# Performance work log

Measured on AMD Instinct MI355X. Metric: run time of the kernel, lower is better.

Reference implementation:

```python
import jax, jax.numpy as jnp
import numpy as np

ALPHA = 0.2  # LeakyReLU negative slope
MASK_VAL = -9e15


def setup_inputs() -> dict:
    key = jax.random.key(0)
    k1, k2, k3, k4 = jax.random.split(key, 4)
    B, N, F_IN = 4, 2048, 256
    H, HD = 8, 32  # out_features = H*HD = 256
    x = jax.random.normal(k1, (B, N, F_IN), dtype=jnp.float32)
    adj = jax.random.randint(k2, (B, N, N), 0, 2, dtype=jnp.int32)
    W = jax.random.normal(k3, (H, F_IN, HD), dtype=jnp.float32) * (1.0 / np.sqrt(F_IN))
    a = jax.random.normal(k4, (H, 2 * HD, 1), dtype=jnp.float32) * 0.1
    return {"x": x, "adj": adj, "W": W, "a": a}


def reference(x, adj, W, a):
    # x: (B,N,F), W: (H,F,D), a: (H,2D,1)
    B, N, _ = x.shape
    H, _, D = W.shape
    Wh = jnp.einsum('bnf,hfd->bhnd', x, W)  # (B,H,N,D)
    # Split additive attention vector: cat([Wh_i, Wh_j]) @ a == Wh_i@a1 + Wh_j@a2
    a1 = a[:, :D, 0]   # (H,D)
    a2 = a[:, D:, 0]   # (H,D)
    s1 = jnp.einsum('bhnd,hd->bhn', Wh, a1)  # source scores
    s2 = jnp.einsum('bhnd,hd->bhn', Wh, a2)  # target scores
    e = jax.nn.leaky_relu(s1[:, :, :, None] + s2[:, :, None, :], negative_slope=ALPHA)  # (B,H,N,N)
    e = jnp.where(adj[:, None, :, :] == 0, MASK_VAL, e)
    attention = jax.nn.softmax(e, axis=-1)  # dropout skipped (eval mode)
    h = jnp.einsum('bhij,bhjd->bhid', attention, Wh)  # (B,H,N,D)
    h = jnp.transpose(h, (0, 2, 1, 3)).reshape(B, N, H * D)
    return jax.nn.elu(h)
```

## Files before the change

kernel.cpp:

```cpp
#include <hip/hip_runtime.h>
#include <hip/hip_bf16.h>

#define ALPHA 0.2f

typedef __attribute__((ext_vector_type(8))) short short8;
typedef __attribute__((ext_vector_type(4))) short s4;
typedef __attribute__((ext_vector_type(8))) _Float16 h8;
typedef __attribute__((ext_vector_type(2))) _Float16 h2v;
typedef __attribute__((ext_vector_type(4))) float f32x4;

static constexpr int B = 4, N = 2048, F = 256, H = 8, D = 32;
static constexpr int SZ_X = B * N * F, SZ_ADJ = B * N * N, SZ_W = H * F * D, SZ_A = H * 2 * D;
static const float C1 = 1.4426950408889634f;
static const float C2 = ALPHA * 1.4426950408889634f;


__device__ __forceinline__ unsigned rne16(unsigned u) {
    return u + 0x7fffu + ((u >> 16) & 1u);
}
__device__ __forceinline__ unsigned pk_rne(float a, float b) {
    return __builtin_amdgcn_perm(rne16(__float_as_uint(b)),
                                 rne16(__float_as_uint(a)), 0x07060302u);
}
__device__ __forceinline__ unsigned h2mul(unsigned a, unsigned b) {
    h2v r = __builtin_bit_cast(h2v, a) * __builtin_bit_cast(h2v, b);
    return __builtin_bit_cast(unsigned, r);
}
__device__ __forceinline__ unsigned h2max(unsigned a, unsigned b) {
    h2v r = __builtin_elementwise_max(__builtin_bit_cast(h2v, a),
                                      __builtin_bit_cast(h2v, b));
    return __builtin_bit_cast(unsigned, r);
}
__device__ __forceinline__ unsigned dup16f(float x) {
    unsigned short w = __builtin_bit_cast(unsigned short, (_Float16)x);
    return (unsigned)w | ((unsigned)w << 16);
}

__global__ void k0_prep(const float* __restrict__ Wp, const float* __restrict__ ap,
                        unsigned short* __restrict__ WT2, float* __restrict__ AF) {
    int bid = blockIdx.x;
    int h = bid >> 5, d = bid & 31;
    int f = threadIdx.x;
    unsigned short v = (unsigned short)(rne16(__float_as_uint(Wp[(h * F + f) * D + d])) >> 16);
    WT2[(size_t)(f >> 5) * 8192 + (h * 32 + d) * 32 + (f & 31)] = v;
    if (d == 0 && f < 64) AF[h * 64 + f] = ap[h * 64 + f];
}

__global__ void kbit(const int* __restrict__ adj, unsigned long long* __restrict__ bm) {
    int wid = blockIdx.x * 4 + (threadIdx.x >> 6);
    int lane = threadIdx.x & 63;
    size_t base = (size_t)wid * 16;
#pragma unroll
    for (int s = 0; s < 16; s++) {
        size_t strip = base + s;
        int v = adj[strip * 64 + lane];
        unsigned long long m = __ballot(v != 0);
        if (lane == 0) bm[strip] = m;
    }
}

__global__ __launch_bounds__(256) void k12(const float* __restrict__ x,
                                           const unsigned short* __restrict__ WT2,
                                           const float* __restrict__ AF,
                                           unsigned short* __restrict__ WHT,
                                           float* __restrict__ S1,
                                           _Float16* __restrict__ UH,
                                           _Float16* __restrict__ VH) {
    __shared__ unsigned short XA[16 * 264];
    int bid = blockIdx.x;
    int b = bid >> 7;
    int n0 = (bid & 127) * 16;
    int t = threadIdx.x;
    int wave = t >> 6, lane = t & 63;
    int lm = lane & 15, lq = lane >> 4;

#pragma unroll
    for (int q = 0; q < 4; q++) {
        int idx = q * 256 + t;
        int row = idx >> 6, c16 = idx & 63;
        f32x4 v = *(const f32x4*)(x + (size_t)(b * N + n0 + row) * F + c16 * 4);
        unsigned* dst = (unsigned*)&XA[row * 264 + c16 * 4];
        dst[0] = pk_rne(v[0], v[1]);
        dst[1] = pk_rne(v[2], v[3]);
    }
    __syncthreads();

    f32x4 acc[4] = {};
#pragma unroll
    for (int kc = 0; kc < 8; kc++) {
        short8 afr = *(const short8*)&XA[lm * 264 + kc * 32 + lq * 8];
#pragma unroll
        for (int c = 0; c < 4; c++) {
            int hd = wave * 64 + c * 16 + lm;
            short8 bfr = *(const short8*)(WT2 + (size_t)kc * 8192 + hd * 32 + lq * 8);
            acc[c] = __builtin_amdgcn_mfma_f32_16x16x32_bf16(afr, bfr, acc[c], 0, 0, 0);
        }
    }

#pragma unroll
    for (int c = 0; c < 4; c++) {
        int hd = wave * 64 + c * 16 + lm;
        unsigned short w0 = __builtin_bit_cast(unsigned short, (_Float16)acc[c][0]);
        unsigned short w1 = __builtin_bit_cast(unsigned short, (_Float16)acc[c][1]);
        unsigned short w2 = __builtin_bit_cast(unsigned short, (_Float16)acc[c][2]);
        unsigned short w3 = __builtin_bit_cast(unsigned short, (_Float16)acc[c][3]);
        uint2 pk;
        pk.x = (unsigned)w0 | ((unsigned)w1 << 16);
        pk.y = (unsigned)w2 | ((unsigned)w3 << 16);
        *(uint2*)&WHT[((size_t)b * 256 + hd) * 2048 + n0 + lq * 4] = pk;
    }
#pragma unroll
    for (int cp = 0; cp < 2; cp++) {
        int h = wave * 2 + cp;
        float a1l = AF[h * 64 + lm],      a1h = AF[h * 64 + 16 + lm];
        float a2l = AF[h * 64 + 32 + lm], a2h = AF[h * 64 + 48 + lm];
#pragma unroll
        for (int r = 0; r < 4; r++) {
            float s1p = acc[cp * 2][r] * a1l + acc[cp * 2 + 1][r] * a1h;
            float s2p = acc[cp * 2][r] * a2l + acc[cp * 2 + 1][r] * a2h;
#pragma unroll
            for (int off = 1; off <= 8; off <<= 1) {
                s1p += __shfl_xor(s1p, off);
                s2p += __shfl_xor(s2p, off);
            }
            if (lm == 0) {
                int bh = b * 8 + h, n = n0 + lq * 4 + r;
                S1[(size_t)bh * 2048 + n] = s1p;
                UH[(size_t)bh * 2048 + n] = (_Float16)exp2f(C1 * s2p);
                VH[(size_t)bh * 2048 + n] = (_Float16)exp2f(C2 * s2p);
            }
        }
    }
}

__global__ __launch_bounds__(256) void k3_attn(
    const unsigned* __restrict__ bm32,
    const unsigned short* __restrict__ WHT,
    const float* __restrict__ S1,
    const _Float16* __restrict__ UH, const _Float16* __restrict__ VH,
    float* __restrict__ out) {
    __shared__ unsigned LM[4][32 * 66];
    __shared__ unsigned short LW[2][32 * 140];

    int bid = blockIdx.x;
    int isup = bid & 15;
    int bh = bid >> 4;
    int b = bh >> 3, h = bh & 7;
    int i0 = isup * 128;
    int t = threadIdx.x;
    int wave = t >> 6, lane = t & 63;
    int irow = lane & 15, quad = lane >> 4;
    int iw = i0 + wave * 32;

    {
        unsigned* lm = LM[wave];
        const unsigned* src = bm32 + ((size_t)(b * N + iw)) * 64;
#pragma unroll 4
        for (int r = 0; r < 32; r++)
            lm[r * 66 + lane] = src[(size_t)r * 64 + lane];
    }

    const unsigned short* wsrc = WHT + ((size_t)b * 256 + h * 32) * 2048;
    int srow = t >> 3, sseg = (t & 7) * 16;

    {
        const unsigned short* g = wsrc + (size_t)srow * 2048 + sseg;
        union { short8 v; s4 q[2]; } a, c;
        a.v = *(const short8*)(g);
        c.v = *(const short8*)(g + 8);
        unsigned short* d = &LW[0][srow * 140 + sseg];
        *(s4*)(d) = a.q[0]; *(s4*)(d + 4) = a.q[1];
        *(s4*)(d + 8) = c.q[0]; *(s4*)(d + 12) = c.q[1];
    }

    float s1A = S1[(size_t)bh * 2048 + iw + irow];
    float s1B = S1[(size_t)bh * 2048 + iw + 16 + irow];
    unsigned ci2A = dup16f(exp2f((C2 - C1) * s1A));
    unsigned ci2B = dup16f(exp2f((C2 - C1) * s1B));
    const _Float16* up = UH + (size_t)bh * 2048;
    const _Float16* vp = VH + (size_t)bh * 2048;

    union { h8 v; unsigned u[4]; } ones;
    ones.u[0] = ones.u[1] = ones.u[2] = ones.u[3] = 0x3C003C00u;

    f32x4 aA0 = {0,0,0,0}, aA1 = {0,0,0,0}, aAL = {0,0,0,0};
    f32x4 aB0 = {0,0,0,0}, aB1 = {0,0,0,0}, aBL = {0,0,0,0};
    __syncthreads();

    for (int cc = 0; cc < 16; cc++) {
        union { short8 v; s4 q[2]; } pa, pc;
        if (cc < 15) {
            const unsigned short* g = wsrc + (size_t)srow * 2048 + (cc + 1) * 128 + sseg;
            pa.v = *(const short8*)(g);
            pc.v = *(const short8*)(g + 8);
        }
        const unsigned short* lwp = LW[cc & 1];
        const unsigned* lmw = LM[wave];
#pragma unroll
        for (int ks = 0; ks < 4; ks++) {
            int jl = ks * 32 + quad * 8;
            int jg = cc * 128 + jl;
            uint4 uw = *(const uint4*)(up + jg);
            uint4 vw = *(const uint4*)(vp + jg);
            unsigned mkA = lmw[irow * 66 + cc * 4 + ks] >> (quad * 8);
            unsigned mkB = lmw[(16 + irow) * 66 + cc * 4 + ks] >> (quad * 8);
            unsigned mA0 = ((mkA & 1u)  ? 0x3C00u : 0u) | ((mkA & 2u)   ? 0x3C000000u : 0u);
            unsigned mA1 = ((mkA & 4u)  ? 0x3C00u : 0u) | ((mkA & 8u)   ? 0x3C000000u : 0u);
            unsigned mA2 = ((mkA & 16u) ? 0x3C00u : 0u) | ((mkA & 32u)  ? 0x3C000000u : 0u);
            unsigned mA3 = ((mkA & 64u) ? 0x3C00u : 0u) | ((mkA & 128u) ? 0x3C000000u : 0u);
            unsigned mB0 = ((mkB & 1u)  ? 0x3C00u : 0u) | ((mkB & 2u)   ? 0x3C000000u : 0u);
            unsigned mB1 = ((mkB & 4u)  ? 0x3C00u : 0u) | ((mkB & 8u)   ? 0x3C000000u : 0u);
            unsigned mB2 = ((mkB & 16u) ? 0x3C00u : 0u) | ((mkB & 32u)  ? 0x3C000000u : 0u);
            unsigned mB3 = ((mkB & 64u) ? 0x3C00u : 0u) | ((mkB & 128u) ? 0x3C000000u : 0u);
            union { h8 v; unsigned u[4]; } afA, afB;
            afA.u[0] = h2mul(h2max(uw.x, h2mul(ci2A, vw.x)), mA0);
            afA.u[1] = h2mul(h2max(uw.y, h2mul(ci2A, vw.y)), mA1);
            afA.u[2] = h2mul(h2max(uw.z, h2mul(ci2A, vw.z)), mA2);
            afA.u[3] = h2mul(h2max(uw.w, h2mul(ci2A, vw.w)), mA3);
            afB.u[0] = h2mul(h2max(uw.x, h2mul(ci2B, vw.x)), mB0);
            afB.u[1] = h2mul(h2max(uw.y, h2mul(ci2B, vw.y)), mB1);
            afB.u[2] = h2mul(h2max(uw.z, h2mul(ci2B, vw.z)), mB2);
            afB.u[3] = h2mul(h2max(uw.w, h2mul(ci2B, vw.w)), mB3);
            union { short8 v; s4 q[2]; } bf0, bf1;
            bf0.q[0] = *(const s4*)&lwp[irow * 140 + jl];
            bf0.q[1] = *(const s4*)&lwp[irow * 140 + jl + 4];
            bf1.q[0] = *(const s4*)&lwp[(16 + irow) * 140 + jl];
            bf1.q[1] = *(const s4*)&lwp[(16 + irow) * 140 + jl + 4];
            h8 b0 = __builtin_bit_cast(h8, bf0.v);
            h8 b1 = __builtin_bit_cast(h8, bf1.v);
            aA0 = __builtin_amdgcn_mfma_f32_16x16x32_f16(afA.v, b0, aA0, 0, 0, 0);
            aA1 = __builtin_amdgcn_mfma_f32_16x16x32_f16(afA.v, b1, aA1, 0, 0, 0);
            aAL = __builtin_amdgcn_mfma_f32_16x16x32_f16(afA.v, ones.v, aAL, 0, 0, 0);
            aB0 = __builtin_amdgcn_mfma_f32_16x16x32_f16(afB.v, b0, aB0, 0, 0, 0);
            aB1 = __builtin_amdgcn_mfma_f32_16x16x32_f16(afB.v, b1, aB1, 0, 0, 0);
            aBL = __builtin_amdgcn_mfma_f32_16x16x32_f16(afB.v, ones.v, aBL, 0, 0, 0);
        }
        if (cc < 15) {
            unsigned short* d = &LW[(cc + 1) & 1][srow * 140 + sseg];
            *(s4*)(d) = pa.q[0]; *(s4*)(d + 4) = pa.q[1];
            *(s4*)(d + 8) = pc.q[0]; *(s4*)(d + 12) = pc.q[1];
        }
        __syncthreads();
    }

#pragma unroll
    for (int r = 0; r < 4; r++) {
        float lA = aAL[r], lB = aBL[r];
        float rA = 1.0f / (lA > 0.f ? lA : 1.f);
        float rB = 1.0f / (lB > 0.f ? lB : 1.f);
        float vA0 = aA0[r] * rA, vA1 = aA1[r] * rA;
        float vB0 = aB0[r] * rB, vB1 = aB1[r] * rB;
        vA0 = vA0 > 0.f ? vA0 : __expf(vA0) - 1.f;
        vA1 = vA1 > 0.f ? vA1 : __expf(vA1) - 1.f;
        vB0 = vB0 > 0.f ? vB0 : __expf(vB0) - 1.f;
        vB1 = vB1 > 0.f ? vB1 : __expf(vB1) - 1.f;
        int iA = iw + quad * 4 + r, iB = iA + 16;
        size_t rbA = (size_t)(b * N + iA) * 256 + h * 32;
        size_t rbB = (size_t)(b * N + iB) * 256 + h * 32;
        out[rbA + irow] = vA0;
        out[rbA + 16 + irow] = vA1;
        out[rbB + irow] = vB0;
        out[rbB + 16 + irow] = vB1;
    }
}

extern "C" void kernel_launch(void* const* d_in, const int* in_sizes, int n_in,
                              void* d_out, int out_size, void* d_ws, size_t ws_size,
                              hipStream_t stream) {
    const void *xP = nullptr, *adjP = nullptr, *WP = nullptr, *aP = nullptr;
    for (int i = 0; i < n_in; i++) {
        switch (in_sizes[i]) {
            case SZ_X:   xP = d_in[i]; break;
            case SZ_ADJ: adjP = d_in[i]; break;
            case SZ_W:   WP = d_in[i]; break;
            case SZ_A:   aP = d_in[i]; break;
            default: break;
        }
    }
    if (!xP || !adjP || !WP || !aP) { xP = d_in[0]; adjP = d_in[1]; WP = d_in[2]; aP = d_in[3]; }
    float* out = (float*)d_out;

    char* ws = (char*)d_ws;
    unsigned short* WT2 = (unsigned short*)(ws);
    float* AF  = (float*)(ws + 131072);
    float* S1  = (float*)(ws + 133120);
    _Float16* UH = (_Float16*)(ws + 395264);
    _Float16* VH = (_Float16*)(ws + 526336);
    unsigned short* WHT = (unsigned short*)(ws + 657408);
    unsigned long long* BM = (unsigned long long*)(ws + 4851712);

    k0_prep<<<256, 256, 0, stream>>>((const float*)WP, (const float*)aP, WT2, AF);
    kbit<<<4096, 256, 0, stream>>>((const int*)adjP, BM);
    k12<<<512, 256, 0, stream>>>((const float*)xP, WT2, AF, WHT, S1, UH, VH);
    k3_attn<<<512, 256, 0, stream>>>((const unsigned*)BM, WHT, S1, UH, VH, out);
}
```

Baseline: 155.3 us.

## Fuse adjacency bitmask pass into projection kernel, bitwise mask, remap attention blocks

Merges the adjacency-to-bitmask kernel and the projection/score kernel into a single launch, interleaving eight bitmask blocks with one projection block so the memory-bound and compute-bound work overlap and one launch is saved. In the attention loop, the per-pair mask multiply is replaced by a bitwise AND against a mask built with a multiply and arithmetic shift, which removes several selects and one fp16 multiply per element. The attention block index is remapped so consecutive blocks cover different heads of the same batch, aiming at better L2 reuse of the bitmask rows. The mixed-role grid gives blocks uneven work, which can hurt scheduling balance.

```diff
diff --git a/kernel.cpp b/kernel.cpp
--- a/kernel.cpp
+++ b/kernel.cpp
@@ -8,6 +8,7 @@
 typedef __attribute__((ext_vector_type(8))) _Float16 h8;
 typedef __attribute__((ext_vector_type(2))) _Float16 h2v;
 typedef __attribute__((ext_vector_type(4))) float f32x4;
+typedef __attribute__((ext_vector_type(2))) short sh2;
 
 static constexpr int B = 4, N = 2048, F = 256, H = 8, D = 32;
 static constexpr int SZ_X = B * N * F, SZ_ADJ = B * N * N, SZ_W = H * F * D, SZ_A = H * 2 * D;
@@ -34,6 +35,12 @@
 __device__ __forceinline__ unsigned dup16f(float x) {
     unsigned short w = __builtin_bit_cast(unsigned short, (_Float16)x);
     return (unsigned)w | ((unsigned)w << 16);
+}
+__device__ __forceinline__ unsigned bits2mask(unsigned mk, unsigned mulc) {
+    unsigned w = (mk & 3u) * mulc;
+    sh2 s = __builtin_bit_cast(sh2, w);
+    s = s >> 15;
+    return __builtin_bit_cast(unsigned, s);
 }
 
 __global__ void k0_prep(const float* __restrict__ Wp, const float* __restrict__ ap,
@@ -46,31 +53,37 @@
     if (d == 0 && f < 64) AF[h * 64 + f] = ap[h * 64 + f];
 }
 
-__global__ void kbit(const int* __restrict__ adj, unsigned long long* __restrict__ bm) {
-    int wid = blockIdx.x * 4 + (threadIdx.x >> 6);
-    int lane = threadIdx.x & 63;
-    size_t base = (size_t)wid * 16;
-#pragma unroll
-    for (int s = 0; s < 16; s++) {
-        size_t strip = base + s;
-        int v = adj[strip * 64 + lane];
-        unsigned long long m = __ballot(v != 0);
-        if (lane == 0) bm[strip] = m;
-    }
-}
-
-__global__ __launch_bounds__(256) void k12(const float* __restrict__ x,
-                                           const unsigned short* __restrict__ WT2,
-                                           const float* __restrict__ AF,
-                                           unsigned short* __restrict__ WHT,
-                                           float* __restrict__ S1,
-                                           _Float16* __restrict__ UH,
-                                           _Float16* __restrict__ VH) {
+__global__ __launch_bounds__(256) void k2_fused(const float* __restrict__ x,
+                                                const unsigned short* __restrict__ WT2,
+                                                const float* __restrict__ AF,
+                                                unsigned short* __restrict__ WHT,
+                                                float* __restrict__ S1,
+                                                _Float16* __restrict__ UH,
+                                                _Float16* __restrict__ VH,
+                                                const int* __restrict__ adj,
+                                                unsigned long long* __restrict__ bm) {
     __shared__ unsigned short XA[16 * 264];
     int bid = blockIdx.x;
-    int b = bid >> 7;
-    int n0 = (bid & 127) * 16;
+    int rr = bid % 9;
+    int grp = bid / 9;
     int t = threadIdx.x;
+
+    if (rr != 8) {
+        int wid = (grp * 8 + rr) * 4 + (t >> 6);
+        int lane = t & 63;
+        size_t base = (size_t)wid * 16;
+#pragma unroll
+        for (int s = 0; s < 16; s++) {
+            size_t strip = base + s;
+            int v = adj[strip * 64 + lane];
+            unsigned long long m = __ballot(v != 0);
+            if (lane == 0) bm[strip] = m;
+        }
+        return;
+    }
+
+    int b = grp >> 7;
+    int n0 = (grp & 127) * 16;
     int wave = t >> 6, lane = t & 63;
     int lm = lane & 15, lq = lane >> 4;
 
@@ -143,8 +156,8 @@
     __shared__ unsigned short LW[2][32 * 140];
 
     int bid = blockIdx.x;
-    int isup = bid & 15;
-    int bh = bid >> 4;
+    int bh = (bid & 7) + ((bid >> 7) << 3);
+    int isup = (bid >> 3) & 15;
     int b = bh >> 3, h = bh & 7;
     int i0 = isup * 128;
     int t = threadIdx.x;
@@ -153,11 +166,11 @@
     int iw = i0 + wave * 32;
 
     {
-        unsigned* lm = LM[wave];
+        unsigned* lmp = LM[wave];
         const unsigned* src = bm32 + ((size_t)(b * N + iw)) * 64;
 #pragma unroll 4
         for (int r = 0; r < 32; r++)
-            lm[r * 66 + lane] = src[(size_t)r * 64 + lane];
+            lmp[r * 66 + lane] = src[(size_t)r * 64 + lane];
     }
 
     const unsigned short* wsrc = WHT + ((size_t)b * 256 + h * 32) * 2048;
@@ -183,6 +196,8 @@
     union { h8 v; unsigned u[4]; } ones;
     ones.u[0] = ones.u[1] = ones.u[2] = ones.u[3] = 0x3C003C00u;
 
+    const unsigned MUL = 0x40008000u;
+
     f32x4 aA0 = {0,0,0,0}, aA1 = {0,0,0,0}, aAL = {0,0,0,0};
     f32x4 aB0 = {0,0,0,0}, aB1 = {0,0,0,0}, aBL = {0,0,0,0};
     __syncthreads();
@@ -204,23 +219,23 @@
             uint4 vw = *(const uint4*)(vp + jg);
             unsigned mkA = lmw[irow * 66 + cc * 4 + ks] >> (quad * 8);
             unsigned mkB = lmw[(16 + irow) * 66 + cc * 4 + ks] >> (quad * 8);
-            unsigned mA0 = ((mkA & 1u)  ? 0x3C00u : 0u) | ((mkA & 2u)   ? 0x3C000000u : 0u);
-            unsigned mA1 = ((mkA & 4u)  ? 0x3C00u : 0u) | ((mkA & 8u)   ? 0x3C000000u : 0u);
-            unsigned mA2 = ((mkA & 16u) ? 0x3C00u : 0u) | ((mkA & 32u)  ? 0x3C000000u : 0u);
-            unsigned mA3 = ((mkA & 64u) ? 0x3C00u : 0u) | ((mkA & 128u) ? 0x3C000000u : 0u);
-            unsigned mB0 = ((mkB & 1u)  ? 0x3C00u : 0u) | ((mkB & 2u)   ? 0x3C000000u : 0u);
-            unsigned mB1 = ((mkB & 4u)  ? 0x3C00u : 0u) | ((mkB & 8u)   ? 0x3C000000u : 0u);
-            unsigned mB2 = ((mkB & 16u) ? 0x3C00u : 0u) | ((mkB & 32u)  ? 0x3C000000u : 0u);
-            unsigned mB3 = ((mkB & 64u) ? 0x3C00u : 0u) | ((mkB & 128u) ? 0x3C000000u : 0u);
+            unsigned mA0 = bits2mask(mkA,      MUL);
+            unsigned mA1 = bits2mask(mkA >> 2, MUL);
+            unsigned mA2 = bits2mask(mkA >> 4, MUL);
+            unsigned mA3 = bits2mask(mkA >> 6, MUL);
+            unsigned mB0 = bits2mask(mkB,      MUL);
+            unsigned mB1 = bits2mask(mkB >> 2, MUL);
+            unsigned mB2 = bits2mask(mkB >> 4, MUL);
+            unsigned mB3 = bits2mask(mkB >> 6, MUL);
             union { h8 v; unsigned u[4]; } afA, afB;
-            afA.u[0] = h2mul(h2max(uw.x, h2mul(ci2A, vw.x)), mA0);
-            afA.u[1] = h2mul(h2max(uw.y, h2mul(ci2A, vw.y)), mA1);
-            afA.u[2] = h2mul(h2max(uw.z, h2mul(ci2A, vw.z)), mA2);
-            afA.u[3] = h2mul(h2max(uw.w, h2mul(ci2A, vw.w)), mA3);
-            afB.u[0] = h2mul(h2max(uw.x, h2mul(ci2B, vw.x)), mB0);
-            afB.u[1] = h2mul(h2max(uw.y, h2mul(ci2B, vw.y)), mB1);
-            afB.u[2] = h2mul(h2max(uw.z, h2mul(ci2B, vw.z)), mB2);
-            afB.u[3] = h2mul(h2max(uw.w, h2mul(ci2B, vw.w)), mB3);
+            afA.u[0] = h2max(uw.x, h2mul(ci2A, vw.x)) & mA0;
+            afA.u[1] = h2max(uw.y, h2mul(ci2A, vw.y)) & mA1;
+            afA.u[2] = h2max(uw.z, h2mul(ci2A, vw.z)) & mA2;
+            afA.u[3] = h2max(uw.w, h2mul(ci2A, vw.w)) & mA3;
+            afB.u[0] = h2max(uw.x, h2mul(ci2B, vw.x)) & mB0;
+            afB.u[1] = h2max(uw.y, h2mul(ci2B, vw.y)) & mB1;
+            afB.u[2] = h2max(uw.z, h2mul(ci2B, vw.z)) & mB2;
+            afB.u[3] = h2max(uw.w, h2mul(ci2B, vw.w)) & mB3;
             union { short8 v; s4 q[2]; } bf0, bf1;
             bf0.q[0] = *(const s4*)&lwp[irow * 140 + jl];
             bf0.q[1] = *(const s4*)&lwp[irow * 140 + jl + 4];
@@ -290,7 +305,7 @@
     unsigned long long* BM = (unsigned long long*)(ws + 4851712);
 
     k0_prep<<<256, 256, 0, stream>>>((const float*)WP, (const float*)aP, WT2, AF);
-    kbit<<<4096, 256, 0, stream>>>((const int*)adjP, BM);
-    k12<<<512, 256, 0, stream>>>((const float*)xP, WT2, AF, WHT, S1, UH, VH);
+    k2_fused<<<4608, 256, 0, stream>>>((const float*)xP, WT2, AF, WHT, S1, UH, VH,
+                                       (const int*)adjP, BM);
     k3_attn<<<512, 256, 0, stream>>>((const unsigned*)BM, WHT, S1, UH, VH, out);
 }
```

Result: no change. 157.2 us (+1.2%).
